# Kernel tuning notes

Hardware: AMD Instinct MI355X
Metric: run time of the kernel (lower is better)

Reference implementation:

```python
import jax, jax.numpy as jnp
import numpy as np


def setup_inputs() -> dict:
    key = jax.random.key(0)
    ks = jax.random.split(key, 10)
    B, C, D, H, W = 2, 512, 8, 32, 32
    Ck = C // 4  # shared KV head dim (and fixed query dim per intended MQA math)
    s = 0.02
    return {
        "x": jax.random.normal(ks[0], (B, C, D, H, W), dtype=jnp.float32),
        "Wq": jax.random.normal(ks[1], (Ck, C), dtype=jnp.float32) * s,
        "bq": jnp.zeros((Ck,), dtype=jnp.float32),
        "Wk": jax.random.normal(ks[2], (Ck, C), dtype=jnp.float32) * s,
        "bk": jnp.zeros((Ck,), dtype=jnp.float32),
        "Wv": jax.random.normal(ks[3], (Ck, C), dtype=jnp.float32) * s,
        "bv": jnp.zeros((Ck,), dtype=jnp.float32),
        "Wo": jax.random.normal(ks[4], (C, C), dtype=jnp.float32) * s,
        "bo": jnp.zeros((C,), dtype=jnp.float32),
    }


def reference(x, Wq, bq, Wk, bk, Wv, bv, Wo, bo):
    B, C, D, H, W = x.shape
    N = D * H * W
    Ck = Wk.shape[0]  # C // 4
    xf = x.reshape(B, C, N)  # flatten spatial dims -> sequence axis
    # 1x1 Conv3d == per-voxel linear projection over channels
    q = jnp.einsum('oc,bcn->bno', Wq, xf) + bq  # [B, N, Ck]
    k = jnp.einsum('oc,bcn->bno', Wk, xf) + bk  # [B, N, Ck]
    v = jnp.einsum('oc,bcn->bno', Wv, xf) + bv  # [B, N, Ck]
    scale = jnp.asarray(Ck, x.dtype) ** -0.5
    attn = jax.nn.softmax(jnp.einsum('bnc,bmc->bnm', q, k) * scale, axis=-1)  # [B, N, N]
    out = jnp.einsum('bnm,bmc->bnc', attn, v)  # [B, N, Ck]
    out = jnp.tile(out, (1, 1, 4))  # repeat(1,1,4) -> [B, N, C]
    out = jnp.einsum('oc,bnc->bon', Wo, out) + bo[None, :, None]  # [B, C, N]
    return out.reshape(B, C, D, H, W) + x
```

## Files before the change

kernel.cpp:

```cpp
#include <hip/hip_runtime.h>
#include <hip/hip_bf16.h>

typedef __bf16 bf16;
typedef __bf16 bf16x8 __attribute__((ext_vector_type(8)));
typedef __bf16 bf16x4 __attribute__((ext_vector_type(4)));
typedef float  f32x4  __attribute__((ext_vector_type(4)));
typedef float  f32x16 __attribute__((ext_vector_type(16)));
typedef unsigned int u32;
typedef u32 u32x4 __attribute__((ext_vector_type(4)));

constexpr int BB = 2, C = 512, NN = 8192, CK = 128;

__device__ __forceinline__ u32 cvt_pk_bf16(float lo, float hi) {
    u32 r;
    asm("v_cvt_pk_bf16_f32 %0, %1, %2" : "=v"(r) : "v"(lo), "v"(hi));
    return r;
}
__device__ __forceinline__ void pl32_swap(u32& a, u32& b) {
    asm("v_permlane32_swap_b32 %0, %1" : "+v"(a), "+v"(b));
}

__global__ __launch_bounds__(256) void k_qkv(
    const float* __restrict__ x,
    const float* __restrict__ Wq, const float* __restrict__ bq,
    const float* __restrict__ Wk, const float* __restrict__ bk,
    const float* __restrict__ Wv, const float* __restrict__ bv,
    bf16* __restrict__ qkv_ws)
{
    const int t = threadIdx.x;
    const int lane = t & 63, w = t >> 6;
    const int lr = lane & 15, lg = lane >> 4;

    const int lin = blockIdx.x;
    const int rid = (lin & 7) * 48 + (lin >> 3);
    const int n0 = (rid / 6) * 128;
    const int sub = rid % 6;
    const int which = sub >> 1;
    const int b = sub & 1;

    const float* W    = which == 0 ? Wq : (which == 1 ? Wk : Wv);
    const float* bias = which == 0 ? bq : (which == 1 ? bk : bv);
    bf16* out = qkv_ws + (size_t)which * BB * NN * CK;

    __shared__ __align__(16) char s_xT[128 * 144];
    __shared__ __align__(16) char s_w [128 * 144];

    f32x4 acc[2][8];
#pragma unroll
    for (int m = 0; m < 2; m++)
#pragma unroll
        for (int j = 0; j < 8; j++) acc[m][j] = (f32x4){0.f, 0.f, 0.f, 0.f};

    const float* xb = x + (size_t)b * C * NN;

    const int tok4 = (t & 31) * 4;
    const int c8   = (t >> 5) * 8;
    const int ob   = t >> 2;
    const int c16  = (t & 3) * 16;

    for (int kt = 0; kt < C; kt += 64) {
        __syncthreads();
        {
            float4 v[8];
#pragma unroll
            for (int i = 0; i < 8; i++)
                v[i] = *(const float4*)(xb + (size_t)(kt + c8 + i) * NN + n0 + tok4);
#pragma unroll
            for (int j = 0; j < 4; j++) {
                int tok = tok4 + j;
                bf16x8 pk = { (bf16)v[0].x, (bf16)v[1].x, (bf16)v[2].x, (bf16)v[3].x,
                              (bf16)v[4].x, (bf16)v[5].x, (bf16)v[6].x, (bf16)v[7].x };
                if (j == 1) pk = (bf16x8){ (bf16)v[0].y, (bf16)v[1].y, (bf16)v[2].y, (bf16)v[3].y,
                                           (bf16)v[4].y, (bf16)v[5].y, (bf16)v[6].y, (bf16)v[7].y };
                if (j == 2) pk = (bf16x8){ (bf16)v[0].z, (bf16)v[1].z, (bf16)v[2].z, (bf16)v[3].z,
                                           (bf16)v[4].z, (bf16)v[5].z, (bf16)v[6].z, (bf16)v[7].z };
                if (j == 3) pk = (bf16x8){ (bf16)v[0].w, (bf16)v[1].w, (bf16)v[2].w, (bf16)v[3].w,
                                           (bf16)v[4].w, (bf16)v[5].w, (bf16)v[6].w, (bf16)v[7].w };
                int off = tok * 144 + ((c8 * 2) ^ ((((tok >> 2) & 7)) << 4));
                *(bf16x8*)(s_xT + off) = pk;
            }
        }
#pragma unroll
        for (int p = 0; p < 2; p++) {
            int o = ob + p * 64;
            const float* wp = W + (size_t)o * C + kt + c16;
            float4 a0 = *(const float4*)(wp);
            float4 a1 = *(const float4*)(wp + 4);
            float4 a2 = *(const float4*)(wp + 8);
            float4 a3 = *(const float4*)(wp + 12);
            bf16x8 p0 = { (bf16)a0.x, (bf16)a0.y, (bf16)a0.z, (bf16)a0.w,
                          (bf16)a1.x, (bf16)a1.y, (bf16)a1.z, (bf16)a1.w };
            bf16x8 p1 = { (bf16)a2.x, (bf16)a2.y, (bf16)a2.z, (bf16)a2.w,
                          (bf16)a3.x, (bf16)a3.y, (bf16)a3.z, (bf16)a3.w };
            int perm = ((o >> 2) & 7) << 4;
            *(bf16x8*)(s_w + o * 144 + ((c16 * 2) ^ perm)) = p0;
            *(bf16x8*)(s_w + o * 144 + ((c16 * 2 + 16) ^ perm)) = p1;
        }
        __syncthreads();
#pragma unroll
        for (int ks = 0; ks < 2; ks++) {
            bf16x8 af[2];
#pragma unroll
            for (int m = 0; m < 2; m++) {
                int row = w * 32 + m * 16 + lr;
                af[m] = *(const bf16x8*)(s_xT + row * 144 + ((ks * 64 + lg * 16) ^ ((((row >> 2) & 7)) << 4)));
            }
#pragma unroll
            for (int j = 0; j < 8; j++) {
                int row = j * 16 + lr;
                bf16x8 bfr = *(const bf16x8*)(s_w + row * 144 + ((ks * 64 + lg * 16) ^ ((((row >> 2) & 7)) << 4)));
                acc[0][j] = __builtin_amdgcn_mfma_f32_16x16x32_bf16(af[0], bfr, acc[0][j], 0, 0, 0);
                acc[1][j] = __builtin_amdgcn_mfma_f32_16x16x32_bf16(af[1], bfr, acc[1][j], 0, 0, 0);
            }
        }
    }
#pragma unroll
    for (int m = 0; m < 2; m++)
#pragma unroll
        for (int j = 0; j < 8; j++) {
            int o = j * 16 + lr;
            float bia = bias[o];
#pragma unroll
            for (int r = 0; r < 4; r++) {
                int tok = n0 + w * 32 + m * 16 + lg * 4 + r;
                out[((size_t)b * NN + tok) * CK + o] = (bf16)(acc[m][j][r] + bia);
            }
        }
}

__global__ __launch_bounds__(512, 2) void k_attn(
    const bf16* __restrict__ qkv_ws,
    float* __restrict__ Opart, float* __restrict__ Lw,
    int nsplit)
{
    const int t = threadIdx.x;
    const int lane = t & 63, w = t >> 6;
    const int lq = lane & 31, hi = lane >> 5;
    const int phase = (w >> 2) & 1;

    const int total = 32 * BB * nsplit;
    const int chunkv = total >> 3;
    const int lin = blockIdx.x;
    const int rid = (lin & 7) * chunkv + (lin >> 3);
    const int qt = rid & 31;
    const int bs = rid >> 5;
    const int b = bs & 1, split = bs >> 1;

    const int q0 = qt * 256;
    const int kbeg = split * (NN / nsplit);
    const int nt = (NN / nsplit) / 64;

    const bf16* kg = qkv_ws + (size_t)BB * NN * CK;
    const bf16* vg = qkv_ws + (size_t)2 * BB * NN * CK;

    __shared__ __align__(16) char s_k[2][64 * 256];
    __shared__ __align__(16) char s_vt[3][128 * 128];

    const int kb0 = lq * 256 + ((((lq & 7) ^ hi)) << 4);
    int vbs[4];
#pragma unroll
    for (int db = 0; db < 4; db++) {
        int d = db * 32 + lq;
        vbs[db] = d * 128 + (((((d ^ (d >> 3)) & 7) ^ hi)) << 4);
    }
    const int t2 = t & 255;
    const int sc = t2 & 15, sr = t2 >> 4;
    const int kw_base = (sr * 256 + sc * 16) ^ ((sr & 7) << 4);
    const int vw_base = (sc * 1024 + sr * 8) ^ ((sc & 7) << 4);

    bf16x8 qf[8];
    {
        const float qs = 0.08838834764831845f * 1.4426950408889634f;
        const bf16* qp = qkv_ws + ((size_t)b * NN + q0 + w * 32 + lq) * CK + hi * 8;
#pragma unroll
        for (int ks = 0; ks < 8; ks++) {
            bf16x8 v = *(const bf16x8*)(qp + ks * 16);
#pragma unroll
            for (int i = 0; i < 8; i++) qf[ks][i] = (bf16)((float)v[i] * qs);
        }
    }

    f32x16 oacc[4];
#pragma unroll
    for (int db = 0; db < 4; db++)
#pragma unroll
        for (int i = 0; i < 16; i++) oacc[db][i] = 0.f;
    float lrun = 0.f;

    const bf16* kp = kg + ((size_t)b * NN + kbeg + sr) * CK + sc * 8;
    const bf16* vp = vg + ((size_t)b * NN + kbeg + sr * 4) * CK + sc * 8;
    bf16x8 stg[4];

    auto issue_loads = [&]() {
        if (w < 4) {
#pragma unroll
            for (int p = 0; p < 4; p++) stg[p] = *(const bf16x8*)(kp + (size_t)(16 * p) * CK);
        } else {
#pragma unroll
            for (int p = 0; p < 4; p++) stg[p] = *(const bf16x8*)(vp + (size_t)p * CK);
        }
        kp += (size_t)64 * CK;
        vp += (size_t)64 * CK;
    };

    auto write_lds = [&](int kbuf, int vbuf) {
        if (w < 4) {
            char* skw = s_k[kbuf] + kw_base;
#pragma unroll
            for (int p = 0; p < 4; p++)
                *(bf16x8*)(skw + p * 4096) = stg[p];
        } else {
            char* svw = s_vt[vbuf];
#pragma unroll
            for (int i = 0; i < 8; i++) {
                bf16x4 pk = { stg[0][i], stg[1][i], stg[2][i], stg[3][i] };
                *(bf16x4*)(svw + (vw_base ^ (i * 144))) = pk;
            }
        }
    };

    f32x16 sa0, sa1;
    auto do_qkt = [&](const char* sk) {
#pragma unroll
        for (int i = 0; i < 16; i++) { sa0[i] = 0.f; sa1[i] = 0.f; }
#pragma unroll
        for (int ks = 0; ks < 8; ks++) {
            bf16x8 kf0 = *(const bf16x8*)(sk + (kb0 ^ (ks * 32)));
            bf16x8 kf1 = *(const bf16x8*)(sk + ((kb0 ^ (ks * 32)) + 8192));
            sa0 = __builtin_amdgcn_mfma_f32_32x32x16_bf16(kf0, qf[ks], sa0, 0, 0, 0);
            sa1 = __builtin_amdgcn_mfma_f32_32x32x16_bf16(kf1, qf[ks], sa1, 0, 0, 0);
        }
    };

    u32 W0[8], W1[8];
    auto do_softmax = [&]() {
        f32x16 p0, p1;
#pragma unroll
        for (int i = 0; i < 16; i++) { p0[i] = exp2f(sa0[i]); p1[i] = exp2f(sa1[i]); }
        float s0 = ((p0[0] + p0[1]) + (p0[2] + p0[3])) + ((p0[4] + p0[5]) + (p0[6] + p0[7]));
        float s1 = ((p0[8] + p0[9]) + (p0[10] + p0[11])) + ((p0[12] + p0[13]) + (p0[14] + p0[15]));
        float s2 = ((p1[0] + p1[1]) + (p1[2] + p1[3])) + ((p1[4] + p1[5]) + (p1[6] + p1[7]));
        float s3 = ((p1[8] + p1[9]) + (p1[10] + p1[11])) + ((p1[12] + p1[13]) + (p1[14] + p1[15]));
        lrun += (s0 + s1) + (s2 + s3);
#pragma unroll
        for (int j = 0; j < 8; j++) {
            W0[j] = cvt_pk_bf16(p0[2 * j], p0[2 * j + 1]);
            W1[j] = cvt_pk_bf16(p1[2 * j], p1[2 * j + 1]);
        }
        pl32_swap(W0[0], W0[2]); pl32_swap(W0[1], W0[3]);
        pl32_swap(W0[4], W0[6]); pl32_swap(W0[5], W0[7]);
        pl32_swap(W1[0], W1[2]); pl32_swap(W1[1], W1[3]);
        pl32_swap(W1[4], W1[6]); pl32_swap(W1[5], W1[7]);
    };

    auto do_pv = [&](const char* sv) {
#pragma unroll
        for (int s = 0; s < 4; s++) {
            u32x4 fw;
            if (s == 0)      fw = (u32x4){W0[0], W0[1], W0[2], W0[3]};
            else if (s == 1) fw = (u32x4){W0[4], W0[5], W0[6], W0[7]};
            else if (s == 2) fw = (u32x4){W1[0], W1[1], W1[2], W1[3]};
            else             fw = (u32x4){W1[4], W1[5], W1[6], W1[7]};
            bf16x8 pa = __builtin_bit_cast(bf16x8, fw);
            const int coff = (s >> 1) * 64 + (s & 1) * 32;
#pragma unroll
            for (int db = 0; db < 4; db++) {
                bf16x8 vf = *(const bf16x8*)(sv + (vbs[db] ^ coff));
                oacc[db] = __builtin_amdgcn_mfma_f32_32x32x16_bf16(pa, vf, oacc[db], 0, 0, 0);
            }
        }
    };

    issue_loads();
    write_lds(0, 0);
    __syncthreads();
    if (nt > 1) issue_loads();
    __builtin_amdgcn_s_setprio(1);
    do_qkt(s_k[0]);
    __builtin_amdgcn_s_setprio(0);
    if (!phase) do_softmax();

    int vb_w = 1, vb_r = 0;
    for (int it = 1; it < nt; it++) {
        write_lds(it & 1, vb_w);
        __syncthreads();
        if (it + 1 < nt) issue_loads();
        if (phase) do_softmax();
        __builtin_amdgcn_s_setprio(1);
        do_qkt(s_k[it & 1]);
        do_pv(s_vt[vb_r]);
        __builtin_amdgcn_s_setprio(0);
        if (!phase) do_softmax();
        vb_r = vb_w;
        vb_w = vb_w + 1 == 3 ? 0 : vb_w + 1;
    }
    if (phase) do_softmax();
    __builtin_amdgcn_s_setprio(1);
    do_pv(s_vt[vb_r]);
    __builtin_amdgcn_s_setprio(0);

    size_t obase = (((size_t)split * BB + b) * NN + q0 + w * 32);
    float ls = lrun + __shfl_xor(lrun, 32);
    if (lane < 32) {
        Lw[obase + lq] = ls;
    }
#pragma unroll
    for (int r = 0; r < 16; r++) {
        int qrow = (r & 3) + 8 * (r >> 2) + 4 * hi;
        float* op = Opart + (obase + qrow) * CK + lq;
#pragma unroll
        for (int db = 0; db < 4; db++) op[db * 32] = oacc[db][r];
    }
}

__global__ __launch_bounds__(256) void k_combine(
    const float* __restrict__ Opart, const float* __restrict__ Lw,
    bf16* __restrict__ ao, int nsplit)
{
    const int t = threadIdx.x;
    const int b = blockIdx.y;
    const int r0 = blockIdx.x * 64;
    const int d4 = (t & 31) * 4;
#pragma unroll
    for (int p = 0; p < 8; p++) {
        int row = r0 + (t >> 5) + p * 8;
        size_t rbase = (size_t)b * NN + row;
        float L = 0.f;
        float4 acc = {0.f, 0.f, 0.f, 0.f};
        for (int s = 0; s < nsplit; s++) {
            size_t sb = ((size_t)s * BB) * NN + rbase;
            L += Lw[sb];
            float4 v = *(const float4*)(Opart + sb * CK + d4);
            acc.x += v.x; acc.y += v.y;
            acc.z += v.z; acc.w += v.w;
        }
        float inv = 1.f / L;
        bf16x4 o4 = { (bf16)(acc.x * inv), (bf16)(acc.y * inv),
                      (bf16)(acc.z * inv), (bf16)(acc.w * inv) };
        *(bf16x4*)(ao + rbase * CK + d4) = o4;
    }
}

__global__ __launch_bounds__(256) void k_out(
    const float* __restrict__ x, const float* __restrict__ Wo, const float* __restrict__ bo,
    const bf16* __restrict__ ao, float* __restrict__ y)
{
    const int t = threadIdx.x;
    const int lane = t & 63, w = t >> 6;
    const int lr = lane & 15, lg = lane >> 4;
    const int n0 = blockIdx.x * 128;
    const int o0 = blockIdx.y * 64;
    const int b = blockIdx.z;

    __shared__ __align__(16) char s_w[64 * 256];
    __shared__ __align__(16) char s_a[128 * 256];

    {
        int c4 = (t & 31) * 4, rbase = t >> 5;
#pragma unroll
        for (int p = 0; p < 8; p++) {
            int row = rbase + p * 8;
            const float* wp = Wo + (size_t)(o0 + row) * C + c4;
            float4 a0 = *(const float4*)(wp);
            float4 a1 = *(const float4*)(wp + 128);
            float4 a2 = *(const float4*)(wp + 256);
            float4 a3 = *(const float4*)(wp + 384);
            bf16x4 r4 = { (bf16)(a0.x + a1.x + a2.x + a3.x), (bf16)(a0.y + a1.y + a2.y + a3.y),
                          (bf16)(a0.z + a1.z + a2.z + a3.z), (bf16)(a0.w + a1.w + a2.w + a3.w) };
            int off = (row * 256 + c4 * 2) ^ ((row & 7) << 4);
            *(bf16x4*)(s_w + off) = r4;
        }
    }
    {
        int chunk = t & 15, rbase = t >> 4;
#pragma unroll
        for (int p = 0; p < 8; p++) {
            int row = rbase + p * 16;
            bf16x8 v = *(const bf16x8*)(ao + ((size_t)b * NN + n0 + row) * CK + chunk * 8);
            int off = (row * 256 + chunk * 16) ^ ((row & 7) << 4);
            *(bf16x8*)(s_a + off) = v;
        }
    }
    __syncthreads();

    f32x4 acc[8];
#pragma unroll
    for (int j = 0; j < 8; j++) acc[j] = (f32x4){0.f, 0.f, 0.f, 0.f};
#pragma unroll
    for (int ks = 0; ks < 4; ks++) {
        int row = w * 16 + lr;
        int aoff = (row * 256 + (ks * 32 + lg * 8) * 2) ^ ((row & 7) << 4);
        bf16x8 wf = *(const bf16x8*)(s_w + aoff);
#pragma unroll
        for (int j = 0; j < 8; j++) {
            int nrow = j * 16 + lr;
            int boff = (nrow * 256 + (ks * 32 + lg * 8) * 2) ^ ((nrow & 7) << 4);
            bf16x8 af = *(const bf16x8*)(s_a + boff);
            acc[j] = __builtin_amdgcn_mfma_f32_16x16x32_bf16(wf, af, acc[j], 0, 0, 0);
        }
    }
#pragma unroll
    for (int j = 0; j < 8; j++) {
        int n = n0 + j * 16 + lr;
#pragma unroll
        for (int r = 0; r < 4; r++) {
            int o = o0 + w * 16 + lg * 4 + r;
            size_t idx = ((size_t)b * C + o) * NN + n;
            y[idx] = acc[j][r] + bo[o] + x[idx];
        }
    }
}

extern "C" void kernel_launch(void* const* d_in, const int* in_sizes, int n_in,
                              void* d_out, int out_size, void* d_ws, size_t ws_size,
                              hipStream_t stream)
{
    const float* x  = (const float*)d_in[0];
    const float* Wq = (const float*)d_in[1];
    const float* bq = (const float*)d_in[2];
    const float* Wk = (const float*)d_in[3];
    const float* bk = (const float*)d_in[4];
    const float* Wv = (const float*)d_in[5];
    const float* bv = (const float*)d_in[6];
    const float* Wo = (const float*)d_in[7];
    const float* bo = (const float*)d_in[8];
    float* y = (float*)d_out;

    const size_t qkv_elems = (size_t)3 * BB * NN * CK;
    const size_t ao_elems  = (size_t)BB * NN * CK;

    bf16* qkv = (bf16*)d_ws;
    bf16* ao  = qkv + qkv_elems;
    float* Opart = (float*)(ao + ao_elems);

    int nsplit = 4;
    {
        size_t fixed = (qkv_elems + ao_elems) * sizeof(bf16);
        size_t per_split = ((size_t)BB * NN * CK + (size_t)BB * NN) * sizeof(float);
        while (nsplit > 1 && fixed + (size_t)nsplit * per_split > ws_size) nsplit >>= 1;
    }
    float* Lw = Opart + (size_t)nsplit * BB * NN * CK;

    k_qkv<<<dim3(384, 1, 1), 256, 0, stream>>>(x, Wq, bq, Wk, bk, Wv, bv, qkv);
    k_attn<<<dim3(32 * BB * nsplit, 1, 1), 512, 0, stream>>>(qkv, Opart, Lw, nsplit);
    k_combine<<<dim3(NN / 64, BB), 256, 0, stream>>>(Opart, Lw, ao, nsplit);
    k_out<<<dim3(NN / 128, C / 64, BB), 256, 0, stream>>>(x, Wo, bo, ao, y);
}
```

Measured before the change: 143.6 us.

## Fuse split-KV combine into output projection and store partials in bf16

Result: faster. 134.7 us (median of 2 runs) (-6.2%).

```diff
diff --git a/kernel.cpp b/kernel.cpp
--- a/kernel.cpp
+++ b/kernel.cpp
@@ -130,7 +130,7 @@
 
 __global__ __launch_bounds__(512, 2) void k_attn(
     const bf16* __restrict__ qkv_ws,
-    float* __restrict__ Opart, float* __restrict__ Lw,
+    bf16* __restrict__ Opart, float* __restrict__ Lw,
     int nsplit)
 {
     const int t = threadIdx.x;
@@ -307,43 +307,16 @@
 #pragma unroll
     for (int r = 0; r < 16; r++) {
         int qrow = (r & 3) + 8 * (r >> 2) + 4 * hi;
-        float* op = Opart + (obase + qrow) * CK + lq;
-#pragma unroll
-        for (int db = 0; db < 4; db++) op[db * 32] = oacc[db][r];
-    }
-}
-
-__global__ __launch_bounds__(256) void k_combine(
-    const float* __restrict__ Opart, const float* __restrict__ Lw,
-    bf16* __restrict__ ao, int nsplit)
-{
-    const int t = threadIdx.x;
-    const int b = blockIdx.y;
-    const int r0 = blockIdx.x * 64;
-    const int d4 = (t & 31) * 4;
-#pragma unroll
-    for (int p = 0; p < 8; p++) {
-        int row = r0 + (t >> 5) + p * 8;
-        size_t rbase = (size_t)b * NN + row;
-        float L = 0.f;
-        float4 acc = {0.f, 0.f, 0.f, 0.f};
-        for (int s = 0; s < nsplit; s++) {
-            size_t sb = ((size_t)s * BB) * NN + rbase;
-            L += Lw[sb];
-            float4 v = *(const float4*)(Opart + sb * CK + d4);
-            acc.x += v.x; acc.y += v.y;
-            acc.z += v.z; acc.w += v.w;
-        }
-        float inv = 1.f / L;
-        bf16x4 o4 = { (bf16)(acc.x * inv), (bf16)(acc.y * inv),
-                      (bf16)(acc.z * inv), (bf16)(acc.w * inv) };
-        *(bf16x4*)(ao + rbase * CK + d4) = o4;
+        bf16* op = Opart + (obase + qrow) * CK + lq;
+#pragma unroll
+        for (int db = 0; db < 4; db++) op[db * 32] = (bf16)oacc[db][r];
     }
 }
 
 __global__ __launch_bounds__(256) void k_out(
     const float* __restrict__ x, const float* __restrict__ Wo, const float* __restrict__ bo,
-    const bf16* __restrict__ ao, float* __restrict__ y)
+    const bf16* __restrict__ Opart, const float* __restrict__ Lw,
+    float* __restrict__ y, int nsplit)
 {
     const int t = threadIdx.x;
     const int lane = t & 63, w = t >> 6;
@@ -354,7 +327,15 @@
 
     __shared__ __align__(16) char s_w[64 * 256];
     __shared__ __align__(16) char s_a[128 * 256];
-
+    __shared__ float s_linv[128];
+
+    if (t < 128) {
+        int row = n0 + t;
+        float L = 0.f;
+        for (int s = 0; s < nsplit; s++)
+            L += Lw[((size_t)s * BB + b) * NN + row];
+        s_linv[t] = 1.f / L;
+    }
     {
         int c4 = (t & 31) * 4, rbase = t >> 5;
 #pragma unroll
@@ -371,14 +352,27 @@
             *(bf16x4*)(s_w + off) = r4;
         }
     }
+    __syncthreads();
     {
         int chunk = t & 15, rbase = t >> 4;
 #pragma unroll
         for (int p = 0; p < 8; p++) {
             int row = rbase + p * 16;
-            bf16x8 v = *(const bf16x8*)(ao + ((size_t)b * NN + n0 + row) * CK + chunk * 8);
+            float accv[8];
+#pragma unroll
+            for (int i = 0; i < 8; i++) accv[i] = 0.f;
+            for (int s = 0; s < nsplit; s++) {
+                const bf16* op = Opart + (((size_t)s * BB + b) * NN + n0 + row) * CK + chunk * 8;
+                bf16x8 v = *(const bf16x8*)op;
+#pragma unroll
+                for (int i = 0; i < 8; i++) accv[i] += (float)v[i];
+            }
+            float inv = s_linv[row];
+            bf16x8 outv;
+#pragma unroll
+            for (int i = 0; i < 8; i++) outv[i] = (bf16)(accv[i] * inv);
             int off = (row * 256 + chunk * 16) ^ ((row & 7) << 4);
-            *(bf16x8*)(s_a + off) = v;
+            *(bf16x8*)(s_a + off) = outv;
         }
     }
     __syncthreads();
@@ -427,22 +421,19 @@
     float* y = (float*)d_out;
 
     const size_t qkv_elems = (size_t)3 * BB * NN * CK;
-    const size_t ao_elems  = (size_t)BB * NN * CK;
 
     bf16* qkv = (bf16*)d_ws;
-    bf16* ao  = qkv + qkv_elems;
-    float* Opart = (float*)(ao + ao_elems);
+    bf16* Opart = qkv + qkv_elems;
 
     int nsplit = 4;
     {
-        size_t fixed = (qkv_elems + ao_elems) * sizeof(bf16);
-        size_t per_split = ((size_t)BB * NN * CK + (size_t)BB * NN) * sizeof(float);
+        size_t fixed = qkv_elems * sizeof(bf16);
+        size_t per_split = (size_t)BB * NN * CK * sizeof(bf16) + (size_t)BB * NN * sizeof(float);
         while (nsplit > 1 && fixed + (size_t)nsplit * per_split > ws_size) nsplit >>= 1;
     }
-    float* Lw = Opart + (size_t)nsplit * BB * NN * CK;
+    float* Lw = (float*)(Opart + (size_t)nsplit * BB * NN * CK);
 
     k_qkv<<<dim3(384, 1, 1), 256, 0, stream>>>(x, Wq, bq, Wk, bk, Wv, bv, qkv);
     k_attn<<<dim3(32 * BB * nsplit, 1, 1), 512, 0, stream>>>(qkv, Opart, Lw, nsplit);
-    k_combine<<<dim3(NN / 64, BB), 256, 0, stream>>>(Opart, Lw, ao, nsplit);
-    k_out<<<dim3(NN / 128, C / 64, BB), 256, 0, stream>>>(x, Wo, bo, ao, y);
-}
+    k_out<<<dim3(NN / 128, C / 64, BB), 256, 0, stream>>>(x, Wo, bo, Opart, Lw, y, nsplit);
+}
```
